# Kernel tuning notes

Hardware: AMD Instinct MI355X
Metric: run time of the kernel (lower is better)

The kernel has to match this reference:

```python
import jax, jax.numpy as jnp
import numpy as np

EDGE_DROPOUT = 0.1   # init kwarg edge_dropout
TRAINING = True      # init kwarg is_training
N_NODES = 8192
D_FEAT = 512


def setup_inputs() -> dict:
    key = jax.random.key(0)
    x = jax.random.normal(key, (N_NODES, D_FEAT), dtype=jnp.float32)
    return {"x": x, "k": 30}


def _graph_process(x, k):
    # knn_fast: cosine similarity kNN with symmetric degree normalization.
    n = x.shape[0]
    xn = x / jnp.linalg.norm(x, axis=1, keepdims=True)      # F.normalize(x, dim=1)
    sim = xn @ xn.T                                         # [n, n] (torch does this in blocks of 1000; same math)
    vals, inds = jax.lax.top_k(sim, k + 1)                  # [n, k+1]
    rows = jnp.broadcast_to(jnp.arange(n)[:, None], vals.shape).reshape(-1)
    cols = inds.reshape(-1)
    v = vals.reshape(-1)
    norm_row = vals.sum(axis=1)                             # out-degree mass
    norm_col = jnp.zeros(n, vals.dtype).at[cols].add(v)     # in-degree mass (index_add_)
    norm = norm_row + norm_col
    v = v * (norm[rows] ** -0.5) * (norm[cols] ** -0.5)
    # values[torch.isnan(values)] = 0
    v = jnp.where(jnp.isnan(v), jnp.zeros_like(v), v)
    # symmetrize edge list
    rows_ = jnp.concatenate([rows, cols])
    cols_ = jnp.concatenate([cols, rows])
    v_ = jnp.concatenate([v, v])
    v_ = jax.nn.relu(v_)
    if TRAINING and EDGE_DROPOUT > 0.0:
        keep = jax.random.bernoulli(jax.random.key(42), 1.0 - EDGE_DROPOUT, v_.shape)
        v_ = jnp.where(keep, v_ / (1.0 - EDGE_DROPOUT), jnp.zeros_like(v_))
    # sparse_coo_tensor(...).coalesce(): duplicate (i,j) entries sum -> dense scatter-add
    adj = jnp.zeros((n, n), v_.dtype).at[rows_, cols_].add(v_)
    return adj


def reference(x, k):
    return _graph_process(x, k)
```

## Files before the change

### kernel.cpp

```cpp
#include <hip/hip_runtime.h>
#include <cstdint>
#include <cmath>

#define NN 8192
#define DD 512
#define KP1 31
#define HALF_EDGES (NN * KP1)

typedef float f2 __attribute__((ext_vector_type(2)));

__device__ __forceinline__ uint32_t rotl32(uint32_t v, int s) {
  return (v << s) | (v >> (32 - s));
}

__device__ __forceinline__ void threefry2x32_42(uint32_t x0, uint32_t x1,
                                                uint32_t& o0, uint32_t& o1) {
  const uint32_t ks0 = 0u, ks1 = 42u;
  const uint32_t ks2 = 0x1BD11BDAu ^ ks0 ^ ks1;
  x0 += ks0; x1 += ks1;
  x0 += x1; x1 = rotl32(x1, 13); x1 ^= x0;
  x0 += x1; x1 = rotl32(x1, 15); x1 ^= x0;
  x0 += x1; x1 = rotl32(x1, 26); x1 ^= x0;
  x0 += x1; x1 = rotl32(x1, 6);  x1 ^= x0;
  x0 += ks1; x1 += ks2 + 1u;
  x0 += x1; x1 = rotl32(x1, 17); x1 ^= x0;
  x0 += x1; x1 = rotl32(x1, 29); x1 ^= x0;
  x0 += x1; x1 = rotl32(x1, 16); x1 ^= x0;
  x0 += x1; x1 = rotl32(x1, 24); x1 ^= x0;
  x0 += ks2; x1 += ks0 + 2u;
  x0 += x1; x1 = rotl32(x1, 13); x1 ^= x0;
  x0 += x1; x1 = rotl32(x1, 15); x1 ^= x0;
  x0 += x1; x1 = rotl32(x1, 26); x1 ^= x0;
  x0 += x1; x1 = rotl32(x1, 6);  x1 ^= x0;
  x0 += ks0; x1 += ks1 + 3u;
  x0 += x1; x1 = rotl32(x1, 17); x1 ^= x0;
  x0 += x1; x1 = rotl32(x1, 29); x1 ^= x0;
  x0 += x1; x1 = rotl32(x1, 16); x1 ^= x0;
  x0 += x1; x1 = rotl32(x1, 24); x1 ^= x0;
  x0 += ks1; x1 += ks2 + 4u;
  x0 += x1; x1 = rotl32(x1, 13); x1 ^= x0;
  x0 += x1; x1 = rotl32(x1, 15); x1 ^= x0;
  x0 += x1; x1 = rotl32(x1, 26); x1 ^= x0;
  x0 += x1; x1 = rotl32(x1, 6);  x1 ^= x0;
  x0 += ks2; x1 += ks0 + 5u;
  o0 = x0; o1 = x1;
}

__device__ __forceinline__ bool keep_edge(uint32_t e) {
  uint32_t y0, y1;
  threefry2x32_42(0u, e, y0, y1);
  uint32_t bits = y0 ^ y1;
  float u = __uint_as_float((bits >> 9) | 0x3f800000u) - 1.0f;
  return u < 0.9f;
}

__device__ __forceinline__ void gll16(const float4* gsrc, void* lds) {
  __builtin_amdgcn_global_load_lds(
      (const __attribute__((address_space(1))) uint32_t*)gsrc,
      (__attribute__((address_space(3))) uint32_t*)lds, 16, 0, 0);
}

__global__ __launch_bounds__(256) void rownorm_kernel(const float* __restrict__ x,
                                                      float* __restrict__ nrm) {
#pragma clang fp contract(off)
  __shared__ float rowbuf[16][DD];
  __shared__ float partial[16][4];
  int tid = threadIdx.x;
  int rowbase = blockIdx.x * 16;

  for (int p = 0; p < 8; ++p) {
    int f = tid + p * 256;
    int r = f >> 7, k4 = f & 127;
    *(float4*)(&rowbuf[r][k4 << 2]) =
        *(const float4*)(x + (size_t)(rowbase + r) * DD + (k4 << 2));
  }
  __syncthreads();
  if (tid < 64) {
    int r = tid >> 2, q = tid & 3;
    const float* s = &rowbuf[r][q * 128];
    float a0 = s[0]*s[0], a1 = s[1]*s[1], a2 = s[2]*s[2], a3 = s[3]*s[3];
    float a4 = s[4]*s[4], a5 = s[5]*s[5], a6 = s[6]*s[6], a7 = s[7]*s[7];
    for (int i = 8; i < 128; i += 8) {
      a0 += s[i+0]*s[i+0]; a1 += s[i+1]*s[i+1];
      a2 += s[i+2]*s[i+2]; a3 += s[i+3]*s[i+3];
      a4 += s[i+4]*s[i+4]; a5 += s[i+5]*s[i+5];
      a6 += s[i+6]*s[i+6]; a7 += s[i+7]*s[i+7];
    }
    partial[r][q] = ((a0 + a1) + (a2 + a3)) + ((a4 + a5) + (a6 + a7));
  }
  __syncthreads();
  if (tid < 16) {
    float S = (partial[tid][0] + partial[tid][1]) + (partial[tid][2] + partial[tid][3]);
    nrm[rowbase + tid] = sqrtf(S);
  }
}

__global__ __launch_bounds__(256) void xnorm_kernel(const float* __restrict__ x,
                                                    const float* __restrict__ nrm,
                                                    float* __restrict__ xn) {
#pragma clang fp contract(off)
  int idx = blockIdx.x * 256 + threadIdx.x;
  const float4* xv = (const float4*)x;
  float4* xo = (float4*)xn;
  float4 v = xv[idx];
  float n = nrm[idx >> 7];
  v.x = v.x / n; v.y = v.y / n; v.z = v.z / n; v.w = v.w / n;
  xo[idx] = v;
}

__global__ __launch_bounds__(256) void gemm_kernel_pre(const float* __restrict__ x,
                                                       float* __restrict__ out) {
#pragma clang fp contract(off)
  int bid0 = blockIdx.x;
  int bid = (bid0 & 7) * 260 + (bid0 >> 3);
  int by = (int)((129.0f - sqrtf(16641.0f - 8.0f * (float)bid)) * 0.5f);
  while (64 * by - (by * (by - 1)) / 2 > bid) --by;
  while (64 * (by + 1) - ((by + 1) * by) / 2 <= bid) ++by;
  const int bx = by + (bid - (64 * by - (by * (by - 1)) / 2));

  __shared__ __align__(16) char smem[32768];
  float4* AsF4 = (float4*)smem;
  float*  Bs   = (float*)(smem + 16384);

  const int tid = threadIdx.x;
  const int rb = by * 128;
  const int cb = bx * 128;
  const int m = tid & 3;
  const int g = tid >> 2;

  const int lane = tid & 63, wave = tid >> 6;
  const int wr = wave >> 1, wc = wave & 1;
  const int lr = lane >> 3, lc = lane & 7;
  const int r0 = wr * 64 + lr * 8;
  const int c0 = wc * 64 + lc * 8;
  const int r3 = r0 >> 3;

  f2 acc[8][4];
  #pragma unroll
  for (int i = 0; i < 8; ++i)
    #pragma unroll
    for (int jp = 0; jp < 4; ++jp) { acc[i][jp].x = 0.f; acc[i][jp].y = 0.f; }

  const float4* xv = (const float4*)x;
  float4 rbv[2];

  int gr[2], gs[2];
  #pragma unroll
  for (int q = 0; q < 2; ++q) {
    int fi = wave * 128 + q * 64 + lane;
    gr[q] = fi >> 2;
    gs[q] = ((fi & 3) - (gr[q] >> 3)) & 3;
  }

  auto stage_A = [&](int nbuf, int t) {
    #pragma unroll
    for (int q = 0; q < 2; ++q)
      gll16(xv + (size_t)(rb + gr[q]) * 128 + t * 4 + gs[q],
            (void*)(AsF4 + nbuf * 512 + wave * 128 + q * 64));
  };
  auto load_B = [&](int t) {
    #pragma unroll
    for (int p = 0; p < 2; ++p)
      rbv[p] = xv[(size_t)(cb + g + 64 * p) * 128 + t * 4 + m];
  };
  auto write_B = [&](int nbuf) {
    #pragma unroll
    for (int p = 0; p < 2; ++p) {
      int r = g + 64 * p;
      float* bp = Bs + nbuf * 2048 + (4 * m) * 128 + (r ^ (m << 3));
      bp[0]   = rbv[p].x;
      bp[128] = rbv[p].y;
      bp[256] = rbv[p].z;
      bp[384] = rbv[p].w;
    }
  };

  load_B(0);
  write_B(0);
  stage_A(0, 0);
  load_B(1);

  #pragma unroll 1
  for (int t = 0; t < 32; ++t) {
    const int buf = t & 1;
    __syncthreads();
    if (t < 31) {
      stage_A(buf ^ 1, t + 1);
      write_B(buf ^ 1);
      if (t < 30) load_B(t + 2);
    }
    const float4* Ab = AsF4 + buf * 512;
    const float*  Bb = Bs + buf * 2048;
    #pragma unroll
    for (int k4 = 0; k4 < 4; ++k4) {
      float4 av[8];
      const int tA = (k4 + r3) & 3;
      #pragma unroll
      for (int i = 0; i < 8; ++i) av[i] = Ab[(r0 + i) * 4 + tA];
      const int csw = c0 ^ (k4 << 3);
      #pragma unroll
      for (int kk = 0; kk < 4; ++kk) {
        const float* bp = Bb + (4 * k4 + kk) * 128 + csw;
        float4 b0 = *(const float4*)(bp);
        float4 b1 = *(const float4*)(bp + 4);
        f2 bb0 = {b0.x, b0.y};
        f2 bb1 = {b0.z, b0.w};
        f2 bb2 = {b1.x, b1.y};
        f2 bb3 = {b1.z, b1.w};
        #pragma unroll
        for (int i = 0; i < 8; ++i) {
          float a = ((const float*)&av[i])[kk];
          f2 t0 = a * bb0;
          f2 t1 = a * bb1;
          f2 t2 = a * bb2;
          f2 t3 = a * bb3;
          acc[i][0] = acc[i][0] + t0;
          acc[i][1] = acc[i][1] + t1;
          acc[i][2] = acc[i][2] + t2;
          acc[i][3] = acc[i][3] + t3;
        }
      }
    }
  }

  float4* outv = (float4*)out;

  #pragma unroll
  for (int i = 0; i < 8; ++i) {
    #pragma unroll
    for (int h = 0; h < 2; ++h) {
      float4 o;
      o.x = acc[i][2 * h].x;     o.y = acc[i][2 * h].y;
      o.z = acc[i][2 * h + 1].x; o.w = acc[i][2 * h + 1].y;
      outv[(size_t)(rb + r0 + i) * 2048 + ((cb + c0) >> 2) + h] = o;
    }
  }

  if (rb != cb) {
    float* Cs = (float*)smem;
    #pragma unroll 1
    for (int q = 0; q < 4; ++q) {
      __syncthreads();
      if (wr == (q >> 1) && (lr >> 2) == (q & 1)) {
        const int rB = (lr & 3) * 8;
        #pragma unroll
        for (int i = 0; i < 8; ++i) {
          #pragma unroll
          for (int jp = 0; jp < 4; ++jp)
            *(f2*)(Cs + (rB + i) * 130 + wc * 64 + lc * 8 + 2 * jp) = acc[i][jp];
        }
      }
      __syncthreads();
      #pragma unroll
      for (int q2 = 0; q2 < 4; ++q2) {
        int f = tid + q2 * 256;
        int c = f >> 3, t4 = f & 7;
        float4 o;
        o.x = Cs[(4 * t4 + 0) * 130 + c];
        o.y = Cs[(4 * t4 + 1) * 130 + c];
        o.z = Cs[(4 * t4 + 2) * 130 + c];
        o.w = Cs[(4 * t4 + 3) * 130 + c];
        outv[(size_t)(cb + c) * 2048 + ((rb + q * 32) >> 2) + t4] = o;
      }
    }
  }
}

__global__ __launch_bounds__(256, 2) void gemm_kernel_fb(const float* __restrict__ x,
                                                         const float* __restrict__ nrm,
                                                         float* __restrict__ out) {
#pragma clang fp contract(off)
  int bid = blockIdx.x;
  int by = (int)((129.0f - sqrtf(16641.0f - 8.0f * (float)bid)) * 0.5f);
  while (64 * by - (by * (by - 1)) / 2 > bid) --by;
  while (64 * (by + 1) - ((by + 1) * by) / 2 <= bid) ++by;
  const int bx = by + (bid - (64 * by - (by * (by - 1)) / 2));

  extern __shared__ char smem[];
  float4* AsF4 = (float4*)smem;
  float*  Bs   = (float*)(smem + 16384);

  const int tid = threadIdx.x;
  const int rb = by * 128;
  const int cb = bx * 128;
  const int m = tid & 7;
  const int g = tid >> 3;

  float nA[4], nB[4];
  #pragma unroll
  for (int p = 0; p < 4; ++p) {
    nA[p] = nrm[rb + g + 32 * p];
    nB[p] = nrm[cb + g + 32 * p];
  }

  const int lane = tid & 63, wave = tid >> 6;
  const int wr = wave >> 1, wc = wave & 1;
  const int lr = lane >> 3, lc = lane & 7;
  const int r0 = wr * 64 + lr * 8;
  const int c0 = wc * 64 + lc * 8;
  const int r3 = r0 >> 3;

  f2 acc[8][4];
  #pragma unroll
  for (int i = 0; i < 8; ++i)
    #pragma unroll
    for (int jp = 0; jp < 4; ++jp) { acc[i][jp].x = 0.f; acc[i][jp].y = 0.f; }

  const float4* xv = (const float4*)x;
  float4 ra[4], rbv[4];
  #pragma unroll
  for (int p = 0; p < 4; ++p) {
    int r = g + 32 * p;
    ra[p]  = xv[(size_t)(rb + r) * 128 + m];
    rbv[p] = xv[(size_t)(cb + r) * 128 + m];
  }

  for (int kc = 0; kc < 16; ++kc) {
    __syncthreads();
    #pragma unroll
    for (int p = 0; p < 4; ++p) {
      int r = g + 32 * p;
      float4 va = ra[p];
      va.x = va.x / nA[p]; va.y = va.y / nA[p];
      va.z = va.z / nA[p]; va.w = va.w / nA[p];
      AsF4[r * 8 + ((m + (r >> 3)) & 7)] = va;
      float4 vb = rbv[p];
      vb.x = vb.x / nB[p]; vb.y = vb.y / nB[p];
      vb.z = vb.z / nB[p]; vb.w = vb.w / nB[p];
      float* bp = Bs + (4 * m) * 128 + (r ^ (m << 3));
      bp[0]   = vb.x;
      bp[128] = vb.y;
      bp[256] = vb.z;
      bp[384] = vb.w;
    }
    __syncthreads();
    if (kc < 15) {
      #pragma unroll
      for (int p = 0; p < 4; ++p) {
        int r = g + 32 * p;
        ra[p]  = xv[(size_t)(rb + r) * 128 + (kc + 1) * 8 + m];
        rbv[p] = xv[(size_t)(cb + r) * 128 + (kc + 1) * 8 + m];
      }
    }

    #pragma unroll 2
    for (int k4 = 0; k4 < 8; ++k4) {
      float4 av[8];
      const int tA = (k4 + r3) & 7;
      #pragma unroll
      for (int i = 0; i < 8; ++i) av[i] = AsF4[(r0 + i) * 8 + tA];
      float4 b01[8];
      const int csw = c0 ^ (k4 << 3);
      #pragma unroll
      for (int kk = 0; kk < 4; ++kk) {
        const float* bp = Bs + (4 * k4 + kk) * 128 + csw;
        b01[2 * kk]     = *(const float4*)(bp);
        b01[2 * kk + 1] = *(const float4*)(bp + 4);
      }
      #pragma unroll
      for (int kk = 0; kk < 4; ++kk) {
        f2 bb0 = {b01[2 * kk].x,     b01[2 * kk].y};
        f2 bb1 = {b01[2 * kk].z,     b01[2 * kk].w};
        f2 bb2 = {b01[2 * kk + 1].x, b01[2 * kk + 1].y};
        f2 bb3 = {b01[2 * kk + 1].z, b01[2 * kk + 1].w};
        #pragma unroll
        for (int i = 0; i < 8; ++i) {
          float a = ((const float*)&av[i])[kk];
          f2 t0 = a * bb0;
          f2 t1 = a * bb1;
          f2 t2 = a * bb2;
          f2 t3 = a * bb3;
          acc[i][0] = acc[i][0] + t0;
          acc[i][1] = acc[i][1] + t1;
          acc[i][2] = acc[i][2] + t2;
          acc[i][3] = acc[i][3] + t3;
        }
      }
    }
  }

  float4* outv = (float4*)out;
  #pragma unroll
  for (int i = 0; i < 8; ++i) {
    #pragma unroll
    for (int h = 0; h < 2; ++h) {
      float4 o;
      o.x = acc[i][2 * h].x;     o.y = acc[i][2 * h].y;
      o.z = acc[i][2 * h + 1].x; o.w = acc[i][2 * h + 1].y;
      outv[(size_t)(rb + r0 + i) * 2048 + ((cb + c0) >> 2) + h] = o;
    }
  }
  if (rb != cb) {
    float* Cs = (float*)smem;
    #pragma unroll 1
    for (int q = 0; q < 4; ++q) {
      __syncthreads();
      if (wr == (q >> 1) && (lr >> 2) == (q & 1)) {
        const int rB = (lr & 3) * 8;
        #pragma unroll
        for (int i = 0; i < 8; ++i) {
          #pragma unroll
          for (int jp = 0; jp < 4; ++jp)
            *(f2*)(Cs + (rB + i) * 130 + wc * 64 + lc * 8 + 2 * jp) = acc[i][jp];
        }
      }
      __syncthreads();
      #pragma unroll
      for (int q2 = 0; q2 < 4; ++q2) {
        int f = tid + q2 * 256;
        int c = f >> 3, t4 = f & 7;
        float4 o;
        o.x = Cs[(4 * t4 + 0) * 130 + c];
        o.y = Cs[(4 * t4 + 1) * 130 + c];
        o.z = Cs[(4 * t4 + 2) * 130 + c];
        o.w = Cs[(4 * t4 + 3) * 130 + c];
        outv[(size_t)(cb + c) * 2048 + ((rb + q * 32) >> 2) + t4] = o;
      }
    }
  }
}

__global__ __launch_bounds__(256) void topk_kernel(const float* __restrict__ sim,
                                                   float* __restrict__ vals,
                                                   int* __restrict__ inds) {
  const int w = threadIdx.x >> 6;
  const int lane = threadIdx.x & 63;
  const int row = blockIdx.x * 4 + w;

  float kval = -1e30f;
  int   kidx = 0;
  float kmin = -1e30f;

  const float* srow = sim + (size_t)row * NN;
  for (int grp = 0; grp < NN / 64; ++grp) {
    float v = srow[grp * 64 + lane];
    unsigned long long mask = __ballot(v > kmin);
    while (mask) {
      int src = __builtin_ctzll(mask);
      mask &= mask - 1;
      float vv = __shfl(v, src, 64);
      if (vv > kmin) {
        int cc = grp * 64 + src;
        unsigned long long ge = __ballot(kval >= vv) & 0x7FFFFFFFull;
        int pos = __popcll(ge);
        float upv = __shfl_up(kval, 1, 64);
        int   upi = __shfl_up(kidx, 1, 64);
        if (lane < KP1) {
          if (lane == pos) { kval = vv; kidx = cc; }
          else if (lane > pos) { kval = upv; kidx = upi; }
        }
        kmin = __shfl(kval, KP1 - 1, 64);
      }
    }
  }
  if (lane < KP1) {
    vals[(size_t)row * KP1 + lane] = kval;
    inds[row * KP1 + lane] = kidx;
  }
}

__global__ __launch_bounds__(256) void norm_kernel(const float* __restrict__ vals,
                                                   const int* __restrict__ inds,
                                                   float* __restrict__ norm) {
  int i = blockIdx.x * blockDim.x + threadIdx.x;
  if (i >= NN) return;
  float s = 0.f;
  for (int t = 0; t < KP1; ++t) {
    float v = vals[i * KP1 + t];
    s += v;
    atomicAdd(&norm[inds[i * KP1 + t]], v);
  }
  atomicAdd(&norm[i], s);
}

__global__ __launch_bounds__(256) void scatter_kernel(const float* __restrict__ vals,
                                                      const int* __restrict__ inds,
                                                      const float* __restrict__ norm,
                                                      float* __restrict__ out) {
  int e = blockIdx.x * blockDim.x + threadIdx.x;
  if (e >= HALF_EDGES) return;
  int i = e / KP1;
  int c = inds[e];
  float v = vals[e];
  float nv = v * (1.0f / sqrtf(norm[i])) * (1.0f / sqrtf(norm[c]));
  if (isnan(nv)) nv = 0.f;
  nv = fmaxf(nv, 0.f);
  float scaled = nv / 0.9f;
  if (keep_edge((uint32_t)e))
    atomicAdd(out + (size_t)i * NN + c, scaled);
  if (keep_edge((uint32_t)(e + HALF_EDGES)))
    atomicAdd(out + (size_t)c * NN + i, scaled);
}

extern "C" void kernel_launch(void* const* d_in, const int* in_sizes, int n_in,
                              void* d_out, int out_size, void* d_ws, size_t ws_size,
                              hipStream_t stream) {
  (void)in_sizes; (void)n_in;
  const float* x = (const float*)d_in[0];
  float* out = (float*)d_out;

  float* nrm  = (float*)d_ws;
  float* vals = nrm + NN;
  int*   inds = (int*)(vals + HALF_EDGES);
  float* norm = (float*)(inds + HALF_EDGES);
  float* xn   = (float*)((char*)d_ws + (size_t)(2 * 1024 * 1024));
  const bool pre = ws_size >= (size_t)(2 * 1024 * 1024) + (size_t)NN * DD * 4;

  hipLaunchKernelGGL(rownorm_kernel, dim3(NN / 16), dim3(256), 0, stream, x, nrm);
  if (pre) {
    hipLaunchKernelGGL(xnorm_kernel, dim3(NN * DD / 4 / 256), dim3(256), 0, stream,
                       x, nrm, xn);
    hipLaunchKernelGGL(gemm_kernel_pre, dim3(2080), dim3(256), 0, stream,
                       xn, out);
  } else {
    hipLaunchKernelGGL(gemm_kernel_fb, dim3(2080), dim3(256), 32768, stream,
                       x, nrm, out);
  }
  hipLaunchKernelGGL(topk_kernel, dim3(NN / 4), dim3(256), 0, stream,
                     out, vals, inds);
  hipMemsetAsync(norm, 0, NN * sizeof(float), stream);
  hipLaunchKernelGGL(norm_kernel, dim3((NN + 255) / 256), dim3(256), 0, stream,
                     vals, inds, norm);
  hipMemsetAsync(d_out, 0, (size_t)out_size * sizeof(float), stream);
  hipLaunchKernelGGL(scatter_kernel, dim3((HALF_EDGES + 255) / 256), dim3(256), 0, stream,
                     vals, inds, norm, out);
}
```

Measured before the change: 1.133 ms.

## Fuse norm with transpose and use 1024-thread GEMM with pre-transposed B

Adds a kernel that computes row norms, writes the normalized matrix, and also writes a transposed normalized copy in one pass. Adds a new symmetric GEMM with 1024 threads per block and a 4x4 micro-tile per thread. It stages B from the transposed copy with coalesced direct-to-LDS loads and writes the mirrored tile straight to global without an LDS transpose. This path runs only when the workspace is large enough for the extra transposed buffer. It trades per-thread register reuse for more waves and the extra transposed write.

```diff
diff --git a/kernel.cpp b/kernel.cpp
--- a/kernel.cpp
+++ b/kernel.cpp
@@ -108,6 +108,177 @@
   xo[idx] = v;
 }
 
+__global__ __launch_bounds__(256) void normT_kernel(const float* __restrict__ x,
+                                                    float* __restrict__ nrm,
+                                                    float* __restrict__ xn,
+                                                    float* __restrict__ xnt) {
+#pragma clang fp contract(off)
+  __shared__ float rowbuf[16][DD];
+  __shared__ float partial[16][4];
+  __shared__ float snrm[16];
+  int tid = threadIdx.x;
+  int rowbase = blockIdx.x * 16;
+
+  for (int p = 0; p < 8; ++p) {
+    int f = tid + p * 256;
+    int r = f >> 7, k4 = f & 127;
+    *(float4*)(&rowbuf[r][k4 << 2]) =
+        *(const float4*)(x + (size_t)(rowbase + r) * DD + (k4 << 2));
+  }
+  __syncthreads();
+  if (tid < 64) {
+    int r = tid >> 2, q = tid & 3;
+    const float* s = &rowbuf[r][q * 128];
+    float a0 = s[0]*s[0], a1 = s[1]*s[1], a2 = s[2]*s[2], a3 = s[3]*s[3];
+    float a4 = s[4]*s[4], a5 = s[5]*s[5], a6 = s[6]*s[6], a7 = s[7]*s[7];
+    for (int i = 8; i < 128; i += 8) {
+      a0 += s[i+0]*s[i+0]; a1 += s[i+1]*s[i+1];
+      a2 += s[i+2]*s[i+2]; a3 += s[i+3]*s[i+3];
+      a4 += s[i+4]*s[i+4]; a5 += s[i+5]*s[i+5];
+      a6 += s[i+6]*s[i+6]; a7 += s[i+7]*s[i+7];
+    }
+    partial[r][q] = ((a0 + a1) + (a2 + a3)) + ((a4 + a5) + (a6 + a7));
+  }
+  __syncthreads();
+  if (tid < 16) {
+    float S = (partial[tid][0] + partial[tid][1]) + (partial[tid][2] + partial[tid][3]);
+    float n = sqrtf(S);
+    nrm[rowbase + tid] = n;
+    snrm[tid] = n;
+  }
+  __syncthreads();
+  for (int p = 0; p < 8; ++p) {
+    int f = tid + p * 256;
+    int r = f >> 7, k4 = f & 127;
+    float n = snrm[r];
+    float4 v = *(float4*)(&rowbuf[r][k4 << 2]);
+    v.x = v.x / n; v.y = v.y / n; v.z = v.z / n; v.w = v.w / n;
+    *(float4*)(xn + (size_t)(rowbase + r) * DD + (k4 << 2)) = v;
+  }
+  for (int kq = 0; kq < 2; ++kq) {
+    int k = tid * 2 + kq;
+    #pragma unroll
+    for (int rq = 0; rq < 4; ++rq) {
+      float4 o;
+      o.x = rowbuf[rq * 4 + 0][k] / snrm[rq * 4 + 0];
+      o.y = rowbuf[rq * 4 + 1][k] / snrm[rq * 4 + 1];
+      o.z = rowbuf[rq * 4 + 2][k] / snrm[rq * 4 + 2];
+      o.w = rowbuf[rq * 4 + 3][k] / snrm[rq * 4 + 3];
+      *(float4*)(xnt + (size_t)k * NN + rowbase + rq * 4) = o;
+    }
+  }
+}
+
+__global__ __launch_bounds__(1024) void gemm_kernel_pre2(const float* __restrict__ xn,
+                                                         const float* __restrict__ xnt,
+                                                         float* __restrict__ out) {
+#pragma clang fp contract(off)
+  int bid0 = blockIdx.x;
+  int bid = (bid0 & 7) * 260 + (bid0 >> 3);
+  int by = (int)((129.0f - sqrtf(16641.0f - 8.0f * (float)bid)) * 0.5f);
+  while (64 * by - (by * (by - 1)) / 2 > bid) --by;
+  while (64 * (by + 1) - ((by + 1) * by) / 2 <= bid) ++by;
+  const int bx = by + (bid - (64 * by - (by * (by - 1)) / 2));
+
+  __shared__ __align__(16) char smem[32768];
+  float4* AsF4 = (float4*)smem;
+  float*  Bs   = (float*)(smem + 16384);
+
+  const int tid  = threadIdx.x;
+  const int lane = tid & 63, wave = tid >> 6;
+  const int rb = by * 128, cb = bx * 128;
+
+  const int wr = wave >> 2, wc = wave & 3;
+  const int lr = lane >> 3, lc = lane & 7;
+  const int r0 = wr * 32 + lr * 4;
+  const int c0 = wc * 32 + lc * 4;
+
+  f2 acc[4][2];
+  #pragma unroll
+  for (int i = 0; i < 4; ++i) {
+    acc[i][0].x = 0.f; acc[i][0].y = 0.f;
+    acc[i][1].x = 0.f; acc[i][1].y = 0.f;
+  }
+
+  const float4* xv = (const float4*)xn;
+
+  const bool stA = wave < 8;
+  const int fi = (stA ? wave : wave - 8) * 64 + lane;
+  const int gr = fi >> 2;
+  const int gs = ((fi & 3) - (gr >> 3)) & 3;
+  const int kl = (stA ? 0 : (wave - 8) * 2) + (lane >> 5);
+  const int bcol = (lane & 31) * 4;
+
+  auto stage = [&](int nbuf, int t) {
+    if (stA) {
+      gll16(xv + (size_t)(rb + gr) * 128 + t * 4 + gs,
+            (void*)(AsF4 + nbuf * 512 + wave * 64));
+    } else {
+      gll16((const float4*)(xnt + (size_t)(t * 16 + kl) * NN + cb + bcol),
+            (void*)(Bs + nbuf * 2048 + (wave - 8) * 256));
+    }
+  };
+
+  stage(0, 0);
+
+  #pragma unroll 1
+  for (int t = 0; t < 32; ++t) {
+    const int buf = t & 1;
+    __syncthreads();
+    if (t < 31) stage(buf ^ 1, t + 1);
+    const float4* Ab = AsF4 + buf * 512;
+    const float*  Bb = Bs + buf * 2048;
+    #pragma unroll
+    for (int k4 = 0; k4 < 4; ++k4) {
+      float4 av[4];
+      #pragma unroll
+      for (int i = 0; i < 4; ++i) {
+        int r = r0 + i;
+        av[i] = Ab[r * 4 + ((k4 + (r >> 3)) & 3)];
+      }
+      #pragma unroll
+      for (int kk = 0; kk < 4; ++kk) {
+        float4 b = *(const float4*)(Bb + (4 * k4 + kk) * 128 + c0);
+        f2 bb0 = {b.x, b.y};
+        f2 bb1 = {b.z, b.w};
+        #pragma unroll
+        for (int i = 0; i < 4; ++i) {
+          float a = ((const float*)&av[i])[kk];
+          f2 t0 = a * bb0;
+          f2 t1 = a * bb1;
+          acc[i][0] = acc[i][0] + t0;
+          acc[i][1] = acc[i][1] + t1;
+        }
+      }
+    }
+  }
+
+  float4* outv = (float4*)out;
+
+  #pragma unroll
+  for (int i = 0; i < 4; ++i) {
+    float4 o;
+    o.x = acc[i][0].x; o.y = acc[i][0].y;
+    o.z = acc[i][1].x; o.w = acc[i][1].y;
+    outv[(size_t)(rb + r0 + i) * 2048 + ((cb + c0) >> 2)] = o;
+  }
+  if (rb != cb) {
+    #pragma unroll
+    for (int j = 0; j < 4; ++j) {
+      const int jh = j >> 1;
+      float4 o;
+      if (j & 1) {
+        o.x = acc[0][jh].y; o.y = acc[1][jh].y;
+        o.z = acc[2][jh].y; o.w = acc[3][jh].y;
+      } else {
+        o.x = acc[0][jh].x; o.y = acc[1][jh].x;
+        o.z = acc[2][jh].x; o.w = acc[3][jh].x;
+      }
+      outv[(size_t)(cb + c0 + j) * 2048 + ((rb + r0) >> 2)] = o;
+    }
+  }
+}
+
 __global__ __launch_bounds__(256) void gemm_kernel_pre(const float* __restrict__ x,
                                                        float* __restrict__ out) {
 #pragma clang fp contract(off)
@@ -224,7 +395,6 @@
   }
 
   float4* outv = (float4*)out;
-
   #pragma unroll
   for (int i = 0; i < 8; ++i) {
     #pragma unroll
@@ -235,7 +405,6 @@
       outv[(size_t)(rb + r0 + i) * 2048 + ((cb + c0) >> 2) + h] = o;
     }
   }
-
   if (rb != cb) {
     float* Cs = (float*)smem;
     #pragma unroll 1
@@ -504,15 +673,25 @@
   int*   inds = (int*)(vals + HALF_EDGES);
   float* norm = (float*)(inds + HALF_EDGES);
   float* xn   = (float*)((char*)d_ws + (size_t)(2 * 1024 * 1024));
-  const bool pre = ws_size >= (size_t)(2 * 1024 * 1024) + (size_t)NN * DD * 4;
-
-  hipLaunchKernelGGL(rownorm_kernel, dim3(NN / 16), dim3(256), 0, stream, x, nrm);
-  if (pre) {
+  float* xnt  = (float*)((char*)d_ws + (size_t)(2 * 1024 * 1024) + (size_t)NN * DD * 4);
+  const size_t need_pre  = (size_t)(2 * 1024 * 1024) + (size_t)NN * DD * 4;
+  const size_t need_pre2 = need_pre + (size_t)NN * DD * 4;
+  const bool pre2 = ws_size >= need_pre2;
+  const bool pre  = ws_size >= need_pre;
+
+  if (pre2) {
+    hipLaunchKernelGGL(normT_kernel, dim3(NN / 16), dim3(256), 0, stream,
+                       x, nrm, xn, xnt);
+    hipLaunchKernelGGL(gemm_kernel_pre2, dim3(2080), dim3(1024), 0, stream,
+                       xn, xnt, out);
+  } else if (pre) {
+    hipLaunchKernelGGL(rownorm_kernel, dim3(NN / 16), dim3(256), 0, stream, x, nrm);
     hipLaunchKernelGGL(xnorm_kernel, dim3(NN * DD / 4 / 256), dim3(256), 0, stream,
                        x, nrm, xn);
     hipLaunchKernelGGL(gemm_kernel_pre, dim3(2080), dim3(256), 0, stream,
                        xn, out);
   } else {
+    hipLaunchKernelGGL(rownorm_kernel, dim3(NN / 16), dim3(256), 0, stream, x, nrm);
     hipLaunchKernelGGL(gemm_kernel_fb, dim3(2080), dim3(256), 32768, stream,
                        x, nrm, out);
   }
```

After: 1.138 ms. Within noise of the previous version (+0.5%).
